# Performance work log

Measured on AMD Instinct MI355X. Metric: run time of the kernel, lower is better.

Reference implementation:

```python
import jax, jax.numpy as jnp
import numpy as np

FFT_LIST = [32, 64, 128]
C_IN = 64
C_OUT = 96
C_OUT_PER = C_OUT // len(FFT_LIST)  # 32
BASIC = FFT_LIST[1]                 # base kernel defined at fft=64 -> 33 bins
ALPHA = 0.2                         # tf.nn.leaky_relu default


def setup_inputs() -> dict:
    key = jax.random.key(0)
    k1, k2, k3, k4 = jax.random.split(key, 4)
    B, T = 8, 8192
    bins0 = BASIC // 2 + 1
    return {
        "x": jax.random.normal(k1, (B, T, C_IN), dtype=jnp.float32),
        "kernel_r": jax.random.normal(k2, (1, 1, bins0, C_IN * C_OUT_PER), dtype=jnp.float32) * 0.05,
        "kernel_i": jax.random.normal(k3, (1, 1, bins0, C_IN * C_OUT_PER), dtype=jnp.float32) * 0.05,
        "bias_r": jax.random.normal(k4, (C_OUT,), dtype=jnp.float32) * 0.05,
    }


def _resize_bins(k, bins):
    # tf.image.resize on [1, H=1, W=bins0, C]: bilinear along W, half-pixel, no antialias
    if bins == k.shape[2]:
        return k
    return jax.image.resize(k, (1, 1, bins, k.shape[3]), method="linear", antialias=False)


def _leaky(v):
    return jax.nn.leaky_relu(v, negative_slope=ALPHA)


def reference(x, kernel_r, kernel_i, bias_r):
    B, T, _ = x.shape
    xc = jnp.transpose(x, (0, 2, 1))  # [B, C_in, T]
    outs = []
    for fft_n in FFT_LIST:
        frames = T // fft_n
        bins = fft_n // 2 + 1
        # non-overlapping STFT with no window == reshape + rfft
        xf = jnp.fft.rfft(xc.reshape(B, C_IN, frames, fft_n), axis=-1)  # [B, Cin, F, K] complex64
        kr = _resize_bins(kernel_r, bins)
        ki = _resize_bins(kernel_i, bins)
        kern = (kr + 1j * ki).reshape(bins, C_IN, C_OUT_PER).astype(jnp.complex64)  # [K, Cin, Cout]
        # per-frequency-bin complex matmul over c_in (fuses tile+mul+reduce_sum)
        y = jnp.einsum("bcfk,kco->bofk", xf, kern)  # [B, Cout, F, K]
        # act_domain == 'freq': leaky relu on real and imag parts
        y = _leaky(jnp.real(y)) + 1j * _leaky(jnp.imag(y))
        # inverse STFT (step == length, no window) == irfft + reshape
        yt = jnp.fft.irfft(y, n=fft_n, axis=-1)            # [B, Cout, F, fft_n]
        yt = yt.reshape(B, C_OUT_PER, T)                    # [B, Cout, T]
        outs.append(jnp.transpose(yt, (0, 2, 1)))           # [B, T, Cout]
    out = jnp.concatenate(outs, axis=2)                     # [B, T, C_OUT]
    out = out + bias_r                                      # bias_add(real(bias))
    return out
```

## Files before the change

kernel.cpp:

```cpp
#include <hip/hip_runtime.h>
#include <stdint.h>

#define T_SZ 8192
#define NCH 96

typedef __attribute__((ext_vector_type(8))) short s8v;
typedef __attribute__((ext_vector_type(4))) float f4v;

__device__ __forceinline__ float lo_bf(uint32_t u){ return __uint_as_float(u << 16); }
__device__ __forceinline__ float hi_bf(uint32_t u){ return __uint_as_float(u & 0xffff0000u); }
__device__ __forceinline__ uint32_t f2bf(float f){
    uint32_t u = __float_as_uint(f);
    return (u + 0x7fffu + ((u >> 16) & 1u)) >> 16;
}
__device__ __forceinline__ uint32_t pk2(float a, float b){ return f2bf(a) | (f2bf(b) << 16); }

#define WS_TOTAL_PAIRS 235520
#define WD_OFF   942080
#define WD_ELEMS 27264
#define WA_OFF   996608
#define WA_ELEMS 30464
#define WD64_U16  1920
#define WD128_U16 7680
#define WA64_U16  2304
#define WA128_U16 8960
#define SLOT_A   1114112
#define SLOT_C  10485760
#define WS_PIPE 14942208
#define XF32W   1114112
#define XF64W  10485760
#define XF128W 19398656
#define Y32W   28311552
#define Y64W   32768000
#define Y128W  37224448
#define WS_WIDE 41484288

__global__ void prep_full(const float* __restrict__ kr, const float* __restrict__ ki,
                          char* __restrict__ ws)
{
    int idx = blockIdx.x * 256 + threadIdx.x;
    if (idx < WS_TOTAL_PAIRS) {
        int bins, rem = idx;
        if (rem < 17 * 2048)      { bins = 17; }
        else if (rem < 50 * 2048) { bins = 33; rem -= 17 * 2048; }
        else                      { bins = 65; rem -= 50 * 2048; }
        int k = rem >> 11, co = rem & 2047;
        float s  = (k + 0.5f) * (33.0f / bins) - 0.5f;
        float fl = floorf(s);
        float w1 = s - fl;
        int i0 = min(max((int)fl, 0), 32);
        int i1 = min(max((int)fl + 1, 0), 32);
        float r0 = kr[i0 * 2048 + co], r1 = kr[i1 * 2048 + co];
        float q0 = ki[i0 * 2048 + co], q1 = ki[i1 * 2048 + co];
        ((uint32_t*)ws)[idx] = pk2(fmaf(w1, r1 - r0, r0), fmaf(w1, q1 - q0, q0));
        return;
    }
    int e = idx - WS_TOTAL_PAIRS;
    if (e < WD_ELEMS) {
        int N, NP, base;
        if (e < 1920)      { N = 32;  NP = 40;  base = 0; }
        else if (e < 7680) { N = 64;  NP = 72;  base = WD64_U16;  e -= 1920; }
        else               { N = 128; NP = 136; base = WD128_U16; e -= 7680; }
        int m = e / NP, t = e % NP;
        float v = 0.f;
        if (t < N && m < N + 2) {
            float ang = 6.2831853071795864769f * (float)(((m >> 1) * t) & (N - 1)) / (float)N;
            v = (m & 1) ? -sinf(ang) : cosf(ang);
        }
        ((unsigned short*)(ws + WD_OFF))[base + e] = (unsigned short)f2bf(v);
        return;
    }
    e -= WD_ELEMS;
    if (e < WA_ELEMS) {
        int N, S3, base;
        if (e < 2304)      { N = 32;  S3 = 72;  base = 0; }
        else if (e < 8960) { N = 64;  S3 = 104; base = WA64_U16;  e -= 2304; }
        else               { N = 128; S3 = 168; base = WA128_U16; e -= 8960; }
        int t = e / S3, kk = e % S3;
        int BINS = N / 2 + 1;
        float v = 0.f;
        if (kk < BINS) {
            v = cosf(6.2831853071795864769f * (float)((kk * t) & (N - 1)) / (float)N);
        } else if (kk < N + 2) {
            v = -sinf(6.2831853071795864769f * (float)(((kk - BINS) * t) & (N - 1)) / (float)N);
        }
        ((unsigned short*)(ws + WA_OFF))[base + e] = (unsigned short)f2bf(v);
    }
}

__global__ void prep_resize(const float* __restrict__ kr, const float* __restrict__ ki,
                            uint32_t* __restrict__ wsu)
{
    int idx = blockIdx.x * 256 + threadIdx.x;
    if (idx >= WS_TOTAL_PAIRS) return;
    int bins, rem = idx;
    if (rem < 17 * 2048)      { bins = 17; }
    else if (rem < 50 * 2048) { bins = 33; rem -= 17 * 2048; }
    else                      { bins = 65; rem -= 50 * 2048; }
    int k = rem >> 11, co = rem & 2047;
    float s  = (k + 0.5f) * (33.0f / bins) - 0.5f;
    float fl = floorf(s);
    float w1 = s - fl;
    int i0 = min(max((int)fl, 0), 32);
    int i1 = min(max((int)fl + 1, 0), 32);
    float r0 = kr[i0 * 2048 + co], r1 = kr[i1 * 2048 + co];
    float q0 = ki[i0 * 2048 + co], q1 = ki[i1 * 2048 + co];
    wsu[idx] = pk2(fmaf(w1, r1 - r0, r0), fmaf(w1, q1 - q0, q0));
}

__device__ __forceinline__ s8v ldfr(const unsigned short* p, int stride, int row0, int k0){
    int lane = threadIdx.x & 63;
    return *(const s8v*)(p + (row0 + (lane & 15)) * stride + k0 + ((lane >> 4) << 3));
}

template<int N, int F>
__device__ __forceinline__ void k1_body(int bid, char* smem, const float* __restrict__ x,
        const unsigned short* __restrict__ WD, uint32_t* __restrict__ xfp)
{
    constexpr int BINS = N/2+1, FRAMES = 8192/N, BF = 8*FRAMES;
    constexpr int M2 = 2*BINS, MPAD = ((M2+15)/16)*16, NP = N+8;
    constexpr int COLS = F*64, NTT = COLS/16, NTW = NTT/4, MT = MPAD/16, KS = N/32;
    constexpr int BPB = FRAMES/F;

    unsigned short* W  = (unsigned short*)smem;
    unsigned short* xT = W + MPAD*NP;
    const int tid = threadIdx.x;
    const int b = bid / BPB, g = bid % BPB, f0 = g*F;

    for (int e = tid; e < MPAD*NP/8; e += 256)
        *(uint4*)(W + e*8) = *(const uint4*)(WD + e*8);

    const float* xb = x + ((size_t)b*T_SZ + (size_t)f0*N) * 64;
    for (int e = tid; e < F*N*4; e += 256) {
        int c4 = e & 15, q = e >> 4, s = q*4;
        const float* p = xb + (size_t)s*64 + c4*4;
        float4 v0 = *(const float4*)(p);
        float4 v1 = *(const float4*)(p + 64);
        float4 v2 = *(const float4*)(p + 128);
        float4 v3 = *(const float4*)(p + 192);
        int f = s / N, tq = s % N;
        unsigned short* d = xT + (f*64 + c4*4)*NP + tq;
        *(uint2*)(d)        = make_uint2(pk2(v0.x, v1.x), pk2(v2.x, v3.x));
        *(uint2*)(d + NP)   = make_uint2(pk2(v0.y, v1.y), pk2(v2.y, v3.y));
        *(uint2*)(d + 2*NP) = make_uint2(pk2(v0.z, v1.z), pk2(v2.z, v3.z));
        *(uint2*)(d + 3*NP) = make_uint2(pk2(v0.w, v1.w), pk2(v2.w, v3.w));
    }
    __syncthreads();

    const int wv = tid >> 6, lane = tid & 63;
    const int nt0 = wv * NTW, cl = lane & 15, rg = (lane >> 4) * 4;
    f4v acc[MT][NTW];
    #pragma unroll
    for (int mt = 0; mt < MT; ++mt)
        #pragma unroll
        for (int nw = 0; nw < NTW; ++nw) { f4v zz = {0.f,0.f,0.f,0.f}; acc[mt][nw] = zz; }

    for (int ks = 0; ks < KS; ++ks) {
        s8v a[MT];
        #pragma unroll
        for (int mt = 0; mt < MT; ++mt) a[mt] = ldfr(W, NP, mt*16, ks*32);
        #pragma unroll
        for (int nw = 0; nw < NTW; ++nw) {
            s8v bb = ldfr(xT, NP, (nt0+nw)*16, ks*32);
            #pragma unroll
            for (int mt = 0; mt < MT; ++mt)
                acc[mt][nw] = __builtin_amdgcn_mfma_f32_16x16x32_bf16(a[mt], bb, acc[mt][nw], 0, 0, 0);
        }
    }
    #pragma unroll
    for (int mt = 0; mt < MT; ++mt)
      #pragma unroll
      for (int nw = 0; nw < NTW; ++nw) {
        int col = (nt0+nw)*16 + cl, f = col >> 6, c = col & 63;
        size_t bf = (size_t)b*FRAMES + f0 + f;
        #pragma unroll
        for (int r = 0; r < 4; r += 2) {
            int m = mt*16 + rg + r, k = m >> 1;
            if (k < BINS)
                xfp[((size_t)k*BF + bf)*64 + c] = pk2(acc[mt][nw][r], acc[mt][nw][r+1]);
        }
      }
}

template<int N, int NTW>
__device__ __forceinline__ void k1w_branch(const unsigned short* __restrict__ W,
        const unsigned short* __restrict__ xT, uint32_t* __restrict__ xfp, int b, int w)
{
    constexpr int BINS = N/2+1, M2 = 2*BINS, MPAD = ((M2+15)/16)*16;
    constexpr int MT = MPAD/16, KS = N/32, NP = N+8;
    constexpr int F = 128/N, FRAMES = 8192/N, BF = 8*FRAMES;
    const int tid = threadIdx.x, wv = tid >> 6, lane = tid & 63;
    const int nt0 = wv * NTW, cl = lane & 15, kl = (lane >> 4) << 3, rg = (lane >> 4) * 4;

    f4v acc[MT][NTW];
    #pragma unroll
    for (int mt = 0; mt < MT; ++mt)
        #pragma unroll
        for (int nw = 0; nw < NTW; ++nw) { f4v zz = {0.f,0.f,0.f,0.f}; acc[mt][nw] = zz; }

    for (int ks = 0; ks < KS; ++ks) {
        s8v a[MT];
        #pragma unroll
        for (int mt = 0; mt < MT; ++mt) a[mt] = ldfr(W, NP, mt*16, ks*32);
        #pragma unroll
        for (int nw = 0; nw < NTW; ++nw) {
            int rowb = (nt0+nw)*16 + cl;
            s8v bb = *(const s8v*)(xT + (rowb & 63)*136 + (rowb >> 6)*N + ks*32 + kl);
            #pragma unroll
            for (int mt = 0; mt < MT; ++mt)
                acc[mt][nw] = __builtin_amdgcn_mfma_f32_16x16x32_bf16(a[mt], bb, acc[mt][nw], 0, 0, 0);
        }
    }
    #pragma unroll
    for (int mt = 0; mt < MT; ++mt)
      #pragma unroll
      for (int nw = 0; nw < NTW; ++nw) {
        int col = (nt0+nw)*16 + cl, f = col >> 6, c = col & 63;
        size_t bf = (size_t)b*FRAMES + w*F + f;
        #pragma unroll
        for (int r = 0; r < 4; r += 2) {
            int m = mt*16 + rg + r, k = m >> 1;
            if (k < BINS)
                xfp[((size_t)k*BF + bf)*64 + c] = pk2(acc[mt][nw][r], acc[mt][nw][r+1]);
        }
      }
}

__global__ __launch_bounds__(256) void k1w(const float* __restrict__ x, char* __restrict__ ws)
{
    __shared__ __align__(16) char smem[71936];
    unsigned short* xT   = (unsigned short*)smem;
    unsigned short* Wall = xT + 64*136;
    const unsigned short* WD = (const unsigned short*)(ws + WD_OFF);
    const int tid = threadIdx.x, bid = blockIdx.x;
    const int b = bid >> 6, w = bid & 63;

    for (int e = tid; e < WD_ELEMS/8; e += 256)
        *(uint4*)(Wall + e*8) = *(const uint4*)(WD + e*8);

    const float* xb = x + ((size_t)b*T_SZ + (size_t)w*128) * 64;
    for (int e = tid; e < 512; e += 256) {
        int c4 = e & 15, t0 = (e >> 4) * 4;
        const float* p = xb + (size_t)t0*64 + c4*4;
        float4 v0 = *(const float4*)(p);
        float4 v1 = *(const float4*)(p + 64);
        float4 v2 = *(const float4*)(p + 128);
        float4 v3 = *(const float4*)(p + 192);
        unsigned short* d = xT + (c4*4)*136 + t0;
        *(uint2*)(d)         = make_uint2(pk2(v0.x, v1.x), pk2(v2.x, v3.x));
        *(uint2*)(d + 136)   = make_uint2(pk2(v0.y, v1.y), pk2(v2.y, v3.y));
        *(uint2*)(d + 272)   = make_uint2(pk2(v0.z, v1.z), pk2(v2.z, v3.z));
        *(uint2*)(d + 408)   = make_uint2(pk2(v0.w, v1.w), pk2(v2.w, v3.w));
    }
    __syncthreads();

    k1w_branch<32, 4>(Wall,                          xT, (uint32_t*)(ws + XF32W),  b, w);
    k1w_branch<64, 2>(Wall + WD64_U16,               xT, (uint32_t*)(ws + XF64W),  b, w);
    k1w_branch<128,1>(Wall + WD128_U16,              xT, (uint32_t*)(ws + XF128W), b, w);
}

template<int N>
__device__ __forceinline__ void k2_body(int kbin, int mblk, char* smem,
        const uint32_t* __restrict__ wpair, const uint32_t* __restrict__ xfp,
        unsigned short* __restrict__ y2)
{
    constexpr int BINS = N/2+1, FRAMES = 8192/N, BF = 8*FRAMES, M2 = 2*BINS;
    unsigned short* A  = (unsigned short*)smem;
    unsigned short* W2 = A + 128*136;
    const int tid = threadIdx.x;
    const int bf0 = mblk * 128;

    for (int e = tid; e < 2048; e += 256)
        *(uint4*)(A + (e>>4)*136 + (e&15)*8) =
            *((const uint4*)(xfp + ((size_t)kbin*BF + bf0 + (e>>4))*64) + (e & 15));

    for (int e = tid; e < 2048; e += 256) {
        uint32_t pr = wpair[kbin*2048 + e];
        unsigned short krv = (unsigned short)(pr & 0xffffu);
        unsigned short kiv = (unsigned short)(pr >> 16);
        int c = e >> 5, o = e & 31;
        W2[o*136 + 2*c]          = krv;
        W2[o*136 + 2*c + 1]      = (unsigned short)(kiv ^ 0x8000u);
        W2[(32+o)*136 + 2*c]     = kiv;
        W2[(32+o)*136 + 2*c + 1] = krv;
    }
    __syncthreads();

    const int wv = tid >> 6, lane = tid & 63;
    const int mt0 = wv * 2;
    f4v acc[2][4];
    #pragma unroll
    for (int mt = 0; mt < 2; ++mt)
        #pragma unroll
        for (int nt = 0; nt < 4; ++nt) { f4v zz = {0.f,0.f,0.f,0.f}; acc[mt][nt] = zz; }

    for (int ks = 0; ks < 4; ++ks) {
        s8v a0 = ldfr(A, 136, mt0*16, ks*32);
        s8v a1 = ldfr(A, 136, mt0*16 + 16, ks*32);
        #pragma unroll
        for (int nt = 0; nt < 4; ++nt) {
            s8v bb = ldfr(W2, 136, nt*16, ks*32);
            acc[0][nt] = __builtin_amdgcn_mfma_f32_16x16x32_bf16(a0, bb, acc[0][nt], 0, 0, 0);
            acc[1][nt] = __builtin_amdgcn_mfma_f32_16x16x32_bf16(a1, bb, acc[1][nt], 0, 0, 0);
        }
    }
    const float wk = (kbin == 0 || kbin == BINS-1) ? (1.0f/N) : (2.0f/N);
    const int cl = lane & 15, rg = (lane >> 4) * 4;
    #pragma unroll
    for (int mt = 0; mt < 2; ++mt)
      #pragma unroll
      for (int nt = 0; nt < 4; ++nt) {
        int col = nt*16 + cl;
        int kk = (col < 32) ? kbin : BINS + kbin;
        int o = col & 31;
        #pragma unroll
        for (int r = 0; r < 4; ++r) {
            int bf = bf0 + (mt0+mt)*16 + rg + r;
            float v = acc[mt][nt][r];
            v = (v > 0.f) ? v : 0.2f * v;
            y2[((size_t)bf*M2 + kk)*32 + o] = (unsigned short)f2bf(v * wk);
        }
      }
}

template<int N>
__device__ __forceinline__ void k3_body(int bid, char* smem,
        const unsigned short* __restrict__ WA, const unsigned short* __restrict__ y2,
        const float* __restrict__ bias, float* __restrict__ out)
{
    constexpr int BINS = N/2+1, FRAMES = 8192/N, M2 = 2*BINS;
    constexpr int KP = ((M2+31)/32)*32, S3 = KP+8;
    constexpr int FB = (N==32)?8:(N==64)?4:2, NCOLS = FB*32, KS = KP/32;
    constexpr int COFF = (N==32)?0:(N==64)?32:64;

    unsigned short* A  = (unsigned short*)smem;
    unsigned short* Bt = A + N*S3;
    const int tid = threadIdx.x;
    const int b = bid >> 5, fg = bid & 31, f0 = fg * FB;

    for (int e = tid; e < N*S3/8; e += 256)
        *(uint4*)(A + e*8) = *(const uint4*)(WA + e*8);

    for (int e = tid; e < FB*M2*4; e += 256) {
        int f = e / (M2*4), r = e % (M2*4), kk = r >> 2, og = (r & 3)*8;
        size_t bf = (size_t)b*FRAMES + f0 + f;
        uint4 v = *((const uint4*)(y2 + ((size_t)bf*M2 + kk)*32) + (r & 3));
        unsigned short* dst = Bt + (f*32 + og)*S3 + kk;
        const unsigned short* pv = (const unsigned short*)&v;
        #pragma unroll
        for (int j = 0; j < 8; ++j) dst[j*S3] = pv[j];
    }
    __syncthreads();

    const int wv = tid >> 6, lane = tid & 63;
    constexpr int MTW = (N==128)?2:1;
    constexpr int NTW = (N==128)?4:8;
    const int mt0 = (N==128) ? wv*2 : ((N==32) ? (wv & 1) : wv);
    const int nt0 = (N==32) ? (wv >> 1)*8 : 0;

    f4v acc[MTW][NTW];
    #pragma unroll
    for (int i = 0; i < MTW; ++i)
        #pragma unroll
        for (int nw = 0; nw < NTW; ++nw) { f4v zz = {0.f,0.f,0.f,0.f}; acc[i][nw] = zz; }

    for (int ks = 0; ks < KS; ++ks) {
        s8v a[MTW];
        #pragma unroll
        for (int i = 0; i < MTW; ++i) a[i] = ldfr(A, S3, (mt0+i)*16, ks*32);
        #pragma unroll
        for (int nw = 0; nw < NTW; ++nw) {
            s8v bb = ldfr(Bt, S3, (nt0+nw)*16, ks*32);
            #pragma unroll
            for (int i = 0; i < MTW; ++i)
                acc[i][nw] = __builtin_amdgcn_mfma_f32_16x16x32_bf16(a[i], bb, acc[i][nw], 0, 0, 0);
        }
    }
    const int cl = lane & 15, rg = (lane >> 4) * 4;
    #pragma unroll
    for (int nw = 0; nw < NTW; ++nw) {
        int col = (nt0+nw)*16 + cl, f = col >> 5, o = col & 31;
        float bv = bias[COFF + o];
        #pragma unroll
        for (int i = 0; i < MTW; ++i)
            #pragma unroll
            for (int r = 0; r < 4; ++r) {
                int t = (mt0+i)*16 + rg + r;
                out[((size_t)(b*T_SZ + (f0+f)*N + t))*NCH + COFF + o] = acc[i][nw][r] + bv;
            }
    }
}

__global__ __launch_bounds__(256) void k1s32(const float* __restrict__ x, char* __restrict__ ws)
{
    __shared__ __align__(16) char smem[24320];
    k1_body<32,4>(blockIdx.x, smem, x, (const unsigned short*)(ws + WD_OFF),
                  (uint32_t*)(ws + SLOT_A));
}
template<int N>
__global__ __launch_bounds__(256) void k2s(char* __restrict__ ws)
{
    __shared__ __align__(16) char smem[52224];
    constexpr int MB = (8192/N*8)/128;
    constexpr int WSP = (N==32) ? 0 : (N==64) ? 17*2048 : 50*2048;
    k2_body<N>(blockIdx.x / MB, blockIdx.x % MB, smem, (const uint32_t*)ws + WSP,
               (const uint32_t*)(ws + SLOT_A), (unsigned short*)(ws + SLOT_C));
}
__global__ __launch_bounds__(256) void k3s128(char* __restrict__ ws,
        const float* __restrict__ bias, float* __restrict__ out)
{
    __shared__ __align__(16) char smem[64512];
    k3_body<128>(blockIdx.x, smem, (const unsigned short*)(ws + WA_OFF) + WA128_U16,
                 (const unsigned short*)(ws + SLOT_C), bias, out);
}
__global__ __launch_bounds__(256) void mix32(const float* __restrict__ x, char* __restrict__ ws,
        const float* __restrict__ bias, float* __restrict__ out)
{
    __shared__ __align__(16) char smem[48384];
    int bid = blockIdx.x;
    if (bid < 256)
        k3_body<32>(bid, smem, (const unsigned short*)(ws + WA_OFF),
                    (const unsigned short*)(ws + SLOT_C), bias, out);
    else
        k1_body<64,4>(bid - 256, smem, x, (const unsigned short*)(ws + WD_OFF) + WD64_U16,
                      (uint32_t*)(ws + SLOT_A));
}
__global__ __launch_bounds__(256) void mix64(const float* __restrict__ x, char* __restrict__ ws,
        const float* __restrict__ bias, float* __restrict__ out)
{
    __shared__ __align__(16) char smem[73984];
    int bid = blockIdx.x;
    if (bid < 256)
        k3_body<64>(bid, smem, (const unsigned short*)(ws + WA_OFF) + WA64_U16,
                    (const unsigned short*)(ws + SLOT_C), bias, out);
    else
        k1_body<128,2>(bid - 256, smem, x, (const unsigned short*)(ws + WD_OFF) + WD128_U16,
                       (uint32_t*)(ws + SLOT_A));
}
__global__ __launch_bounds__(256) void k2all(char* __restrict__ ws)
{
    __shared__ __align__(16) char smem[52224];
    int bid = blockIdx.x;
    if (bid < 272)
        k2_body<32>(bid >> 4, bid & 15, smem, (const uint32_t*)ws,
                    (const uint32_t*)(ws + XF32W), (unsigned short*)(ws + Y32W));
    else if (bid < 536) {
        int q = bid - 272;
        k2_body<64>(q >> 3, q & 7, smem, (const uint32_t*)ws + 17*2048,
                    (const uint32_t*)(ws + XF64W), (unsigned short*)(ws + Y64W));
    } else {
        int q = bid - 536;
        k2_body<128>(q >> 2, q & 3, smem, (const uint32_t*)ws + 50*2048,
                     (const uint32_t*)(ws + XF128W), (unsigned short*)(ws + Y128W));
    }
}
__global__ __launch_bounds__(256) void k3all(char* __restrict__ ws,
        const float* __restrict__ bias, float* __restrict__ out)
{
    __shared__ __align__(16) char smem[64512];
    int bid = blockIdx.x;
    if (bid < 256)
        k3_body<32>(bid, smem, (const unsigned short*)(ws + WA_OFF),
                    (const unsigned short*)(ws + Y32W), bias, out);
    else if (bid < 512)
        k3_body<64>(bid - 256, smem, (const unsigned short*)(ws + WA_OFF) + WA64_U16,
                    (const unsigned short*)(ws + Y64W), bias, out);
    else
        k3_body<128>(bid - 512, smem, (const unsigned short*)(ws + WA_OFF) + WA128_U16,
                     (const unsigned short*)(ws + Y128W), bias, out);
}

template<int FFT_N, bool USE_WS>
__global__ __launch_bounds__(256, 2)
void stft_fused(const float* __restrict__ x, const float* __restrict__ kr,
                const float* __restrict__ ki, const float* __restrict__ bias,
                const uint32_t* __restrict__ wsu, float* __restrict__ out)
{
    constexpr int CIN = 64, COUT = 32;
    constexpr int BINS = FFT_N / 2 + 1;
    constexpr int NFR  = 128 / FFT_N;
    constexpr int KQ   = (BINS + 3) / 4;
    constexpr int COFF = (FFT_N == 32) ? 0 : (FFT_N == 64) ? 32 : 64;
    constexpr int WSP  = (FFT_N == 32) ? 0 : (FFT_N == 64) ? 17 * 2048 : 50 * 2048;
    constexpr int XSP  = 68;
    constexpr int CP   = 66;
    constexpr int YP   = BINS + 2;
    constexpr int SMEMF = 128 * XSP + 2 * FFT_N + NFR * BINS * CP * 2;

    __shared__ __align__(16) float smem[SMEMF];
    float*  xs  = smem;
    float2* cst = (float2*)(smem + 128 * XSP);
    float2* xf2 = (float2*)(smem + 128 * XSP + 2 * FFT_N);
    float2* Y2  = (float2*)smem;

    const int tid = threadIdx.x;
    const int bid = blockIdx.x;
    const int b = bid >> 6, w = bid & 63;
    const float* xblk = x + (size_t)(b * T_SZ + w * 128) * CIN;

    for (int i = tid; i < 2048; i += 256) {
        float4 v = ((const float4*)xblk)[i];
        int t = i >> 4;
        int c = (i & 15) * 4;
        *(float4*)&xs[t * XSP + c] = v;
    }
    if (tid < FFT_N) {
        float ang = 6.2831853071795864769f * ((float)tid / (float)FFT_N);
        float sv, cv;
        sincosf(ang, &sv, &cv);
        cst[tid] = make_float2(cv, sv);
    }
    __syncthreads();

    constexpr int NT_DFT = NFR * KQ * 16;
    for (int tile = tid; tile < NT_DFT; tile += 256) {
        int cq  = tile & 15;
        int kqf = tile >> 4;
        int kq  = kqf % KQ, f = kqf / KQ;
        int k0  = kq * 4;
        float accr[4][4] = {};
        float acci[4][4] = {};
        int idx[4] = {0, 0, 0, 0};
        const float* xrow = xs + f * FFT_N * XSP + cq * 4;
        for (int t = 0; t < FFT_N; ++t) {
            float4 xv = *(const float4*)(xrow + t * XSP);
            float xc[4] = {xv.x, xv.y, xv.z, xv.w};
            #pragma unroll
            for (int kk = 0; kk < 4; ++kk) {
                float2 tw = cst[idx[kk]];
                idx[kk] = (idx[kk] + k0 + kk) & (FFT_N - 1);
                #pragma unroll
                for (int cc = 0; cc < 4; ++cc) {
                    accr[kk][cc] = fmaf(xc[cc], tw.x, accr[kk][cc]);
                    acci[kk][cc] = fmaf(xc[cc], tw.y, acci[kk][cc]);
                }
            }
        }
        #pragma unroll
        for (int kk = 0; kk < 4; ++kk) {
            int k = k0 + kk;
            if (k < BINS) {
                #pragma unroll
                for (int cc = 0; cc < 4; ++cc)
                    xf2[(f * BINS + k) * CP + cq * 4 + cc] =
                        make_float2(accr[kk][cc], -acci[kk][cc]);
            }
        }
    }
    __syncthreads();

    constexpr int NT_MM = BINS * 8;
    for (int task = tid; task < NT_MM; task += 256) {
        int oq = task & 7, k = task >> 3;
        float2 accY[NFR][4] = {};
        float w1 = 0.f; int i0 = 0, i1 = 0;
        if (!USE_WS) {
            float s  = (k + 0.5f) * (33.0f / BINS) - 0.5f;
            float fl = floorf(s); w1 = s - fl;
            i0 = min(max((int)fl, 0), 32);
            i1 = min(max((int)fl + 1, 0), 32);
        }
        const uint32_t* wp = USE_WS ? (wsu + WSP + k * 2048 + oq * 4) : (const uint32_t*)nullptr;
        for (int c = 0; c < CIN; ++c) {
            float krv[4], kiv[4];
            if (USE_WS) {
                uint4 u = *(const uint4*)(wp + c * 32);
                krv[0] = lo_bf(u.x); kiv[0] = hi_bf(u.x);
                krv[1] = lo_bf(u.y); kiv[1] = hi_bf(u.y);
                krv[2] = lo_bf(u.z); kiv[2] = hi_bf(u.z);
                krv[3] = lo_bf(u.w); kiv[3] = hi_bf(u.w);
            } else {
                const float* p = kr + (size_t)i0 * 2048 + c * 32 + oq * 4;
                const float* q = kr + (size_t)i1 * 2048 + c * 32 + oq * 4;
                float4 r0 = *(const float4*)p, r1 = *(const float4*)q;
                p = ki + (size_t)i0 * 2048 + c * 32 + oq * 4;
                q = ki + (size_t)i1 * 2048 + c * 32 + oq * 4;
                float4 q0 = *(const float4*)p, q1 = *(const float4*)q;
                krv[0] = fmaf(w1, r1.x - r0.x, r0.x); kiv[0] = fmaf(w1, q1.x - q0.x, q0.x);
                krv[1] = fmaf(w1, r1.y - r0.y, r0.y); kiv[1] = fmaf(w1, q1.y - q0.y, q0.y);
                krv[2] = fmaf(w1, r1.z - r0.z, r0.z); kiv[2] = fmaf(w1, q1.z - q0.z, q0.z);
                krv[3] = fmaf(w1, r1.w - r0.w, r0.w); kiv[3] = fmaf(w1, q1.w - q0.w, q0.w);
            }
            #pragma unroll
            for (int f = 0; f < NFR; ++f) {
                float2 xv = xf2[(f * BINS + k) * CP + c];
                #pragma unroll
                for (int jo = 0; jo < 4; ++jo) {
                    accY[f][jo].x += xv.x * krv[jo] - xv.y * kiv[jo];
                    accY[f][jo].y += xv.x * kiv[jo] + xv.y * krv[jo];
                }
            }
        }
        float wk = (k == 0 || k == BINS - 1) ? (1.0f / FFT_N) : (2.0f / FFT_N);
        #pragma unroll
        for (int f = 0; f < NFR; ++f) {
            #pragma unroll
            for (int jo = 0; jo < 4; ++jo) {
                float yr = accY[f][jo].x; yr = (yr > 0.f) ? yr : 0.2f * yr;
                float yi = accY[f][jo].y; yi = (yi > 0.f) ? yi : 0.2f * yi;
                Y2[(f * COUT + oq * 4 + jo) * YP + k] = make_float2(yr * wk, yi * wk);
            }
        }
    }
    __syncthreads();

    {
        int tq = tid >> 3, oq = tid & 7;
        int tg0 = tq * 4;
        int f   = tg0 / FFT_N;
        int tl0 = tg0 % FFT_N;
        float acc[4][4] = {};
        int idx[4] = {0, 0, 0, 0};
        const float2* yb = Y2 + (f * COUT + oq * 4) * YP;
        for (int k = 0; k < BINS; ++k) {
            float2 tw[4];
            #pragma unroll
            for (int j = 0; j < 4; ++j) {
                tw[j] = cst[idx[j]];
                idx[j] = (idx[j] + tl0 + j) & (FFT_N - 1);
            }
            #pragma unroll
            for (int jo = 0; jo < 4; ++jo) {
                float2 yv = yb[jo * YP + k];
                #pragma unroll
                for (int j = 0; j < 4; ++j)
                    acc[j][jo] += yv.x * tw[j].x - yv.y * tw[j].y;
            }
        }
        float4 bv = *(const float4*)(bias + COFF + oq * 4);
        float* ob = out + ((size_t)(b * T_SZ + w * 128 + tg0)) * NCH + COFF + oq * 4;
        #pragma unroll
        for (int j = 0; j < 4; ++j) {
            float4 o4 = make_float4(acc[j][0] + bv.x, acc[j][1] + bv.y,
                                    acc[j][2] + bv.z, acc[j][3] + bv.w);
            *(float4*)(ob + (size_t)j * NCH) = o4;
        }
    }
}

extern "C" void kernel_launch(void* const* d_in, const int* in_sizes, int n_in,
                              void* d_out, int out_size, void* d_ws, size_t ws_size,
                              hipStream_t stream)
{
    (void)in_sizes; (void)n_in; (void)out_size;
    const float* x    = (const float*)d_in[0];
    const float* kr   = (const float*)d_in[1];
    const float* ki   = (const float*)d_in[2];
    const float* bias = (const float*)d_in[3];
    float* out = (float*)d_out;
    char* ws = (char*)d_ws;
    dim3 blk(256);

    if (ws != nullptr && ws_size >= (size_t)WS_WIDE) {
        prep_full<<<dim3(1146), blk, 0, stream>>>(kr, ki, ws);
        k1w   <<<dim3(512), blk, 0, stream>>>(x, ws);
        k2all <<<dim3(796), blk, 0, stream>>>(ws);
        k3all <<<dim3(768), blk, 0, stream>>>(ws, bias, out);
    } else if (ws != nullptr && ws_size >= (size_t)WS_PIPE) {
        prep_full<<<dim3(1146), blk, 0, stream>>>(kr, ki, ws);
        k1s32   <<<dim3(512), blk, 0, stream>>>(x, ws);
        k2s<32> <<<dim3(272), blk, 0, stream>>>(ws);
        mix32   <<<dim3(512), blk, 0, stream>>>(x, ws, bias, out);
        k2s<64> <<<dim3(264), blk, 0, stream>>>(ws);
        mix64   <<<dim3(512), blk, 0, stream>>>(x, ws, bias, out);
        k2s<128><<<dim3(260), blk, 0, stream>>>(ws);
        k3s128  <<<dim3(256), blk, 0, stream>>>(ws, bias, out);
    } else if (ws != nullptr && ws_size >= (size_t)WS_TOTAL_PAIRS * 4) {
        uint32_t* wsu = (uint32_t*)ws;
        prep_resize<<<dim3(920), blk, 0, stream>>>(kr, ki, wsu);
        stft_fused<32,  true><<<dim3(512), blk, 0, stream>>>(x, kr, ki, bias, wsu, out);
        stft_fused<64,  true><<<dim3(512), blk, 0, stream>>>(x, kr, ki, bias, wsu, out);
        stft_fused<128, true><<<dim3(512), blk, 0, stream>>>(x, kr, ki, bias, wsu, out);
    } else {
        stft_fused<32,  false><<<dim3(512), blk, 0, stream>>>(x, kr, ki, bias, nullptr, out);
        stft_fused<64,  false><<<dim3(512), blk, 0, stream>>>(x, kr, ki, bias, nullptr, out);
        stft_fused<128, false><<<dim3(512), blk, 0, stream>>>(x, kr, ki, bias, nullptr, out);
    }
}
```

Before: 49.05 us.

## Pre-expand complex weights into GEMM layout, split k3 N=128 tiles, add occupancy bounds

Measured after the change: 50.37 us. 1.03x slower.

```diff
diff --git a/kernel.cpp b/kernel.cpp
--- a/kernel.cpp
+++ b/kernel.cpp
@@ -16,46 +16,52 @@
 __device__ __forceinline__ uint32_t pk2(float a, float b){ return f2bf(a) | (f2bf(b) << 16); }
 
 #define WS_TOTAL_PAIRS 235520
-#define WD_OFF   942080
-#define WD_ELEMS 27264
-#define WA_OFF   996608
-#define WA_ELEMS 30464
-#define WD64_U16  1920
-#define WD128_U16 7680
-#define WA64_U16  2304
-#define WA128_U16 8960
-#define SLOT_A   1114112
-#define SLOT_C  10485760
-#define WS_PIPE 14942208
-#define XF32W   1114112
-#define XF64W  10485760
-#define XF128W 19398656
-#define Y32W   28311552
-#define Y64W   32768000
-#define Y128W  37224448
-#define WS_WIDE 41484288
+#define WD_OFF    942080
+#define WD_ELEMS  27264
+#define WA_OFF    996608
+#define WA_ELEMS  30464
+#define WD64_U16   1920
+#define WD128_U16  7680
+#define WA64_U16   2304
+#define WA128_U16  8960
+#define WE_OFF   1057536
+#define WE_U32    471040
+#define XF32W    4194304
+#define XF64W   14680064
+#define XF128W  25165824
+#define Y32W    35651584
+#define Y64W    41943040
+#define Y128W   50331648
+#define WS_WIDE 58720256
 
 __global__ void prep_full(const float* __restrict__ kr, const float* __restrict__ ki,
                           char* __restrict__ ws)
 {
     int idx = blockIdx.x * 256 + threadIdx.x;
-    if (idx < WS_TOTAL_PAIRS) {
-        int bins, rem = idx;
-        if (rem < 17 * 2048)      { bins = 17; }
-        else if (rem < 50 * 2048) { bins = 33; rem -= 17 * 2048; }
-        else                      { bins = 65; rem -= 50 * 2048; }
-        int k = rem >> 11, co = rem & 2047;
+    if (idx < WE_U32) {
+        int g = idx >> 12, r = idx & 4095;
+        int row = r >> 6, c = r & 63;
+        int o = row & 31, half = row >> 5;
+        int bins, k;
+        if (g < 17)      { bins = 17; k = g; }
+        else if (g < 50) { bins = 33; k = g - 17; }
+        else             { bins = 65; k = g - 50; }
         float s  = (k + 0.5f) * (33.0f / bins) - 0.5f;
         float fl = floorf(s);
         float w1 = s - fl;
         int i0 = min(max((int)fl, 0), 32);
         int i1 = min(max((int)fl + 1, 0), 32);
+        int co = c * 32 + o;
         float r0 = kr[i0 * 2048 + co], r1 = kr[i1 * 2048 + co];
         float q0 = ki[i0 * 2048 + co], q1 = ki[i1 * 2048 + co];
-        ((uint32_t*)ws)[idx] = pk2(fmaf(w1, r1 - r0, r0), fmaf(w1, q1 - q0, q0));
+        int N = bins * 2 - 2;
+        float wk = (k == 0 || k == bins - 1) ? (1.0f / N) : (2.0f / N);
+        float vr = fmaf(w1, r1 - r0, r0) * wk;
+        float vi = fmaf(w1, q1 - q0, q0) * wk;
+        ((uint32_t*)(ws + WE_OFF))[idx] = half ? pk2(vi, vr) : pk2(vr, -vi);
         return;
     }
-    int e = idx - WS_TOTAL_PAIRS;
+    int e = idx - WE_U32;
     if (e < WD_ELEMS) {
         int N, NP, base;
         if (e < 1920)      { N = 32;  NP = 40;  base = 0; }
@@ -79,11 +85,10 @@
         int t = e / S3, kk = e % S3;
         int BINS = N / 2 + 1;
         float v = 0.f;
-        if (kk < BINS) {
+        if (kk < BINS)
             v = cosf(6.2831853071795864769f * (float)((kk * t) & (N - 1)) / (float)N);
-        } else if (kk < N + 2) {
+        else if (kk < N + 2)
             v = -sinf(6.2831853071795864769f * (float)(((kk - BINS) * t) & (N - 1)) / (float)N);
-        }
         ((unsigned short*)(ws + WA_OFF))[base + e] = (unsigned short)f2bf(v);
     }
 }
@@ -113,75 +118,6 @@
     return *(const s8v*)(p + (row0 + (lane & 15)) * stride + k0 + ((lane >> 4) << 3));
 }
 
-template<int N, int F>
-__device__ __forceinline__ void k1_body(int bid, char* smem, const float* __restrict__ x,
-        const unsigned short* __restrict__ WD, uint32_t* __restrict__ xfp)
-{
-    constexpr int BINS = N/2+1, FRAMES = 8192/N, BF = 8*FRAMES;
-    constexpr int M2 = 2*BINS, MPAD = ((M2+15)/16)*16, NP = N+8;
-    constexpr int COLS = F*64, NTT = COLS/16, NTW = NTT/4, MT = MPAD/16, KS = N/32;
-    constexpr int BPB = FRAMES/F;
-
-    unsigned short* W  = (unsigned short*)smem;
-    unsigned short* xT = W + MPAD*NP;
-    const int tid = threadIdx.x;
-    const int b = bid / BPB, g = bid % BPB, f0 = g*F;
-
-    for (int e = tid; e < MPAD*NP/8; e += 256)
-        *(uint4*)(W + e*8) = *(const uint4*)(WD + e*8);
-
-    const float* xb = x + ((size_t)b*T_SZ + (size_t)f0*N) * 64;
-    for (int e = tid; e < F*N*4; e += 256) {
-        int c4 = e & 15, q = e >> 4, s = q*4;
-        const float* p = xb + (size_t)s*64 + c4*4;
-        float4 v0 = *(const float4*)(p);
-        float4 v1 = *(const float4*)(p + 64);
-        float4 v2 = *(const float4*)(p + 128);
-        float4 v3 = *(const float4*)(p + 192);
-        int f = s / N, tq = s % N;
-        unsigned short* d = xT + (f*64 + c4*4)*NP + tq;
-        *(uint2*)(d)        = make_uint2(pk2(v0.x, v1.x), pk2(v2.x, v3.x));
-        *(uint2*)(d + NP)   = make_uint2(pk2(v0.y, v1.y), pk2(v2.y, v3.y));
-        *(uint2*)(d + 2*NP) = make_uint2(pk2(v0.z, v1.z), pk2(v2.z, v3.z));
-        *(uint2*)(d + 3*NP) = make_uint2(pk2(v0.w, v1.w), pk2(v2.w, v3.w));
-    }
-    __syncthreads();
-
-    const int wv = tid >> 6, lane = tid & 63;
-    const int nt0 = wv * NTW, cl = lane & 15, rg = (lane >> 4) * 4;
-    f4v acc[MT][NTW];
-    #pragma unroll
-    for (int mt = 0; mt < MT; ++mt)
-        #pragma unroll
-        for (int nw = 0; nw < NTW; ++nw) { f4v zz = {0.f,0.f,0.f,0.f}; acc[mt][nw] = zz; }
-
-    for (int ks = 0; ks < KS; ++ks) {
-        s8v a[MT];
-        #pragma unroll
-        for (int mt = 0; mt < MT; ++mt) a[mt] = ldfr(W, NP, mt*16, ks*32);
-        #pragma unroll
-        for (int nw = 0; nw < NTW; ++nw) {
-            s8v bb = ldfr(xT, NP, (nt0+nw)*16, ks*32);
-            #pragma unroll
-            for (int mt = 0; mt < MT; ++mt)
-                acc[mt][nw] = __builtin_amdgcn_mfma_f32_16x16x32_bf16(a[mt], bb, acc[mt][nw], 0, 0, 0);
-        }
-    }
-    #pragma unroll
-    for (int mt = 0; mt < MT; ++mt)
-      #pragma unroll
-      for (int nw = 0; nw < NTW; ++nw) {
-        int col = (nt0+nw)*16 + cl, f = col >> 6, c = col & 63;
-        size_t bf = (size_t)b*FRAMES + f0 + f;
-        #pragma unroll
-        for (int r = 0; r < 4; r += 2) {
-            int m = mt*16 + rg + r, k = m >> 1;
-            if (k < BINS)
-                xfp[((size_t)k*BF + bf)*64 + c] = pk2(acc[mt][nw][r], acc[mt][nw][r+1]);
-        }
-      }
-}
-
 template<int N, int NTW>
 __device__ __forceinline__ void k1w_branch(const unsigned short* __restrict__ W,
         const unsigned short* __restrict__ xT, uint32_t* __restrict__ xfp, int b, int w)
@@ -226,7 +162,7 @@
       }
 }
 
-__global__ __launch_bounds__(256) void k1w(const float* __restrict__ x, char* __restrict__ ws)
+__global__ __launch_bounds__(256, 2) void k1w(const float* __restrict__ x, char* __restrict__ ws)
 {
     __shared__ __align__(16) char smem[71936];
     unsigned short* xT   = (unsigned short*)smem;
@@ -247,24 +183,25 @@
         float4 v2 = *(const float4*)(p + 128);
         float4 v3 = *(const float4*)(p + 192);
         unsigned short* d = xT + (c4*4)*136 + t0;
-        *(uint2*)(d)         = make_uint2(pk2(v0.x, v1.x), pk2(v2.x, v3.x));
-        *(uint2*)(d + 136)   = make_uint2(pk2(v0.y, v1.y), pk2(v2.y, v3.y));
-        *(uint2*)(d + 272)   = make_uint2(pk2(v0.z, v1.z), pk2(v2.z, v3.z));
-        *(uint2*)(d + 408)   = make_uint2(pk2(v0.w, v1.w), pk2(v2.w, v3.w));
+        *(uint2*)(d)       = make_uint2(pk2(v0.x, v1.x), pk2(v2.x, v3.x));
+        *(uint2*)(d + 136) = make_uint2(pk2(v0.y, v1.y), pk2(v2.y, v3.y));
+        *(uint2*)(d + 272) = make_uint2(pk2(v0.z, v1.z), pk2(v2.z, v3.z));
+        *(uint2*)(d + 408) = make_uint2(pk2(v0.w, v1.w), pk2(v2.w, v3.w));
     }
     __syncthreads();
 
-    k1w_branch<32, 4>(Wall,                          xT, (uint32_t*)(ws + XF32W),  b, w);
-    k1w_branch<64, 2>(Wall + WD64_U16,               xT, (uint32_t*)(ws + XF64W),  b, w);
-    k1w_branch<128,1>(Wall + WD128_U16,              xT, (uint32_t*)(ws + XF128W), b, w);
+    k1w_branch<32, 4>(Wall,             xT, (uint32_t*)(ws + XF32W),  b, w);
+    k1w_branch<64, 2>(Wall + WD64_U16,  xT, (uint32_t*)(ws + XF64W),  b, w);
+    k1w_branch<128,1>(Wall + WD128_U16, xT, (uint32_t*)(ws + XF128W), b, w);
 }
 
 template<int N>
 __device__ __forceinline__ void k2_body(int kbin, int mblk, char* smem,
-        const uint32_t* __restrict__ wpair, const uint32_t* __restrict__ xfp,
+        const unsigned short* __restrict__ we, const uint32_t* __restrict__ xfp,
         unsigned short* __restrict__ y2)
 {
     constexpr int BINS = N/2+1, FRAMES = 8192/N, BF = 8*FRAMES, M2 = 2*BINS;
+    constexpr int GOFF = (N==32) ? 0 : (N==64) ? 17 : 50;
     unsigned short* A  = (unsigned short*)smem;
     unsigned short* W2 = A + 128*136;
     const int tid = threadIdx.x;
@@ -274,16 +211,9 @@
         *(uint4*)(A + (e>>4)*136 + (e&15)*8) =
             *((const uint4*)(xfp + ((size_t)kbin*BF + bf0 + (e>>4))*64) + (e & 15));
 
-    for (int e = tid; e < 2048; e += 256) {
-        uint32_t pr = wpair[kbin*2048 + e];
-        unsigned short krv = (unsigned short)(pr & 0xffffu);
-        unsigned short kiv = (unsigned short)(pr >> 16);
-        int c = e >> 5, o = e & 31;
-        W2[o*136 + 2*c]          = krv;
-        W2[o*136 + 2*c + 1]      = (unsigned short)(kiv ^ 0x8000u);
-        W2[(32+o)*136 + 2*c]     = kiv;
-        W2[(32+o)*136 + 2*c + 1] = krv;
-    }
+    const uint4* wsrc = (const uint4*)(we + (size_t)(GOFF + kbin) * 8192);
+    for (int e = tid; e < 1024; e += 256)
+        *(uint4*)(W2 + (e>>4)*136 + (e&15)*8) = wsrc[e];
     __syncthreads();
 
     const int wv = tid >> 6, lane = tid & 63;
@@ -304,7 +234,6 @@
             acc[1][nt] = __builtin_amdgcn_mfma_f32_16x16x32_bf16(a1, bb, acc[1][nt], 0, 0, 0);
         }
     }
-    const float wk = (kbin == 0 || kbin == BINS-1) ? (1.0f/N) : (2.0f/N);
     const int cl = lane & 15, rg = (lane >> 4) * 4;
     #pragma unroll
     for (int mt = 0; mt < 2; ++mt)
@@ -318,28 +247,47 @@
             int bf = bf0 + (mt0+mt)*16 + rg + r;
             float v = acc[mt][nt][r];
             v = (v > 0.f) ? v : 0.2f * v;
-            y2[((size_t)bf*M2 + kk)*32 + o] = (unsigned short)f2bf(v * wk);
+            y2[((size_t)bf*M2 + kk)*32 + o] = (unsigned short)f2bf(v);
         }
       }
 }
 
-template<int N>
-__device__ __forceinline__ void k3_body(int bid, char* smem,
+__global__ __launch_bounds__(256, 3) void k2all(char* __restrict__ ws)
+{
+    __shared__ __align__(16) char smem[52224];
+    const unsigned short* we = (const unsigned short*)(ws + WE_OFF);
+    int bid = blockIdx.x;
+    if (bid < 272)
+        k2_body<32>(bid >> 4, bid & 15, smem, we,
+                    (const uint32_t*)(ws + XF32W), (unsigned short*)(ws + Y32W));
+    else if (bid < 536) {
+        int q = bid - 272;
+        k2_body<64>(q >> 3, q & 7, smem, we,
+                    (const uint32_t*)(ws + XF64W), (unsigned short*)(ws + Y64W));
+    } else {
+        int q = bid - 536;
+        k2_body<128>(q >> 2, q & 3, smem, we,
+                     (const uint32_t*)(ws + XF128W), (unsigned short*)(ws + Y128W));
+    }
+}
+
+template<int N, int TROWS>
+__device__ __forceinline__ void k3_body(int b, int f0, int t0, char* smem,
         const unsigned short* __restrict__ WA, const unsigned short* __restrict__ y2,
         const float* __restrict__ bias, float* __restrict__ out)
 {
     constexpr int BINS = N/2+1, FRAMES = 8192/N, M2 = 2*BINS;
-    constexpr int KP = ((M2+31)/32)*32, S3 = KP+8;
-    constexpr int FB = (N==32)?8:(N==64)?4:2, NCOLS = FB*32, KS = KP/32;
+    constexpr int KP = ((M2+31)/32)*32, S3 = KP+8, KS = KP/32;
+    constexpr int FB = (N==32)?8:(N==64)?4:2;
     constexpr int COFF = (N==32)?0:(N==64)?32:64;
+    constexpr int NTW = (N==128)?4:8;
 
     unsigned short* A  = (unsigned short*)smem;
-    unsigned short* Bt = A + N*S3;
+    unsigned short* Bt = A + TROWS*S3;
     const int tid = threadIdx.x;
-    const int b = bid >> 5, fg = bid & 31, f0 = fg * FB;
-
-    for (int e = tid; e < N*S3/8; e += 256)
-        *(uint4*)(A + e*8) = *(const uint4*)(WA + e*8);
+
+    for (int e = tid; e < TROWS*S3/8; e += 256)
+        *(uint4*)(A + e*8) = *(const uint4*)(WA + t0*S3 + e*8);
 
     for (int e = tid; e < FB*M2*4; e += 256) {
         int f = e / (M2*4), r = e % (M2*4), kk = r >> 2, og = (r & 3)*8;
@@ -353,27 +301,19 @@
     __syncthreads();
 
     const int wv = tid >> 6, lane = tid & 63;
-    constexpr int MTW = (N==128)?2:1;
-    constexpr int NTW = (N==128)?4:8;
-    const int mt0 = (N==128) ? wv*2 : ((N==32) ? (wv & 1) : wv);
+    const int mt0 = (N==32) ? (wv & 1) : wv;
     const int nt0 = (N==32) ? (wv >> 1)*8 : 0;
 
-    f4v acc[MTW][NTW];
+    f4v acc[NTW];
     #pragma unroll
-    for (int i = 0; i < MTW; ++i)
-        #pragma unroll
-        for (int nw = 0; nw < NTW; ++nw) { f4v zz = {0.f,0.f,0.f,0.f}; acc[i][nw] = zz; }
+    for (int nw = 0; nw < NTW; ++nw) { f4v zz = {0.f,0.f,0.f,0.f}; acc[nw] = zz; }
 
     for (int ks = 0; ks < KS; ++ks) {
-        s8v a[MTW];
-        #pragma unroll
-        for (int i = 0; i < MTW; ++i) a[i] = ldfr(A, S3, (mt0+i)*16, ks*32);
+        s8v a = ldfr(A, S3, mt0*16, ks*32);
         #pragma unroll
         for (int nw = 0; nw < NTW; ++nw) {
             s8v bb = ldfr(Bt, S3, (nt0+nw)*16, ks*32);
-            #pragma unroll
-            for (int i = 0; i < MTW; ++i)
-                acc[i][nw] = __builtin_amdgcn_mfma_f32_16x16x32_bf16(a[i], bb, acc[i][nw], 0, 0, 0);
+            acc[nw] = __builtin_amdgcn_mfma_f32_16x16x32_bf16(a, bb, acc[nw], 0, 0, 0);
         }
     }
     const int cl = lane & 15, rg = (lane >> 4) * 4;
@@ -382,92 +322,31 @@
         int col = (nt0+nw)*16 + cl, f = col >> 5, o = col & 31;
         float bv = bias[COFF + o];
         #pragma unroll
-        for (int i = 0; i < MTW; ++i)
-            #pragma unroll
-            for (int r = 0; r < 4; ++r) {
-                int t = (mt0+i)*16 + rg + r;
-                out[((size_t)(b*T_SZ + (f0+f)*N + t))*NCH + COFF + o] = acc[i][nw][r] + bv;
-            }
-    }
-}
-
-__global__ __launch_bounds__(256) void k1s32(const float* __restrict__ x, char* __restrict__ ws)
-{
-    __shared__ __align__(16) char smem[24320];
-    k1_body<32,4>(blockIdx.x, smem, x, (const unsigned short*)(ws + WD_OFF),
-                  (uint32_t*)(ws + SLOT_A));
-}
-template<int N>
-__global__ __launch_bounds__(256) void k2s(char* __restrict__ ws)
-{
-    __shared__ __align__(16) char smem[52224];
-    constexpr int MB = (8192/N*8)/128;
-    constexpr int WSP = (N==32) ? 0 : (N==64) ? 17*2048 : 50*2048;
-    k2_body<N>(blockIdx.x / MB, blockIdx.x % MB, smem, (const uint32_t*)ws + WSP,
-               (const uint32_t*)(ws + SLOT_A), (unsigned short*)(ws + SLOT_C));
-}
-__global__ __launch_bounds__(256) void k3s128(char* __restrict__ ws,
+        for (int r = 0; r < 4; ++r) {
+            int t = t0 + mt0*16 + rg + r;
+            out[((size_t)(b*T_SZ + (f0+f)*N + t))*NCH + COFF + o] = acc[nw][r] + bv;
+        }
+    }
+}
+
+__global__ __launch_bounds__(256, 3) void k3all(char* __restrict__ ws,
         const float* __restrict__ bias, float* __restrict__ out)
 {
-    __shared__ __align__(16) char smem[64512];
-    k3_body<128>(blockIdx.x, smem, (const unsigned short*)(ws + WA_OFF) + WA128_U16,
-                 (const unsigned short*)(ws + SLOT_C), bias, out);
-}
-__global__ __launch_bounds__(256) void mix32(const float* __restrict__ x, char* __restrict__ ws,
-        const float* __restrict__ bias, float* __restrict__ out)
-{
-    __shared__ __align__(16) char smem[48384];
+    __shared__ __align__(16) char smem[43008];
+    const unsigned short* WA = (const unsigned short*)(ws + WA_OFF);
     int bid = blockIdx.x;
     if (bid < 256)
-        k3_body<32>(bid, smem, (const unsigned short*)(ws + WA_OFF),
-                    (const unsigned short*)(ws + SLOT_C), bias, out);
-    else
-        k1_body<64,4>(bid - 256, smem, x, (const unsigned short*)(ws + WD_OFF) + WD64_U16,
-                      (uint32_t*)(ws + SLOT_A));
-}
-__global__ __launch_bounds__(256) void mix64(const float* __restrict__ x, char* __restrict__ ws,
-        const float* __restrict__ bias, float* __restrict__ out)
-{
-    __shared__ __align__(16) char smem[73984];
-    int bid = blockIdx.x;
-    if (bid < 256)
-        k3_body<64>(bid, smem, (const unsigned short*)(ws + WA_OFF) + WA64_U16,
-                    (const unsigned short*)(ws + SLOT_C), bias, out);
-    else
-        k1_body<128,2>(bid - 256, smem, x, (const unsigned short*)(ws + WD_OFF) + WD128_U16,
-                       (uint32_t*)(ws + SLOT_A));
-}
-__global__ __launch_bounds__(256) void k2all(char* __restrict__ ws)
-{
-    __shared__ __align__(16) char smem[52224];
-    int bid = blockIdx.x;
-    if (bid < 272)
-        k2_body<32>(bid >> 4, bid & 15, smem, (const uint32_t*)ws,
-                    (const uint32_t*)(ws + XF32W), (unsigned short*)(ws + Y32W));
-    else if (bid < 536) {
-        int q = bid - 272;
-        k2_body<64>(q >> 3, q & 7, smem, (const uint32_t*)ws + 17*2048,
-                    (const uint32_t*)(ws + XF64W), (unsigned short*)(ws + Y64W));
+        k3_body<32,32>(bid >> 5, (bid & 31)*8, 0, smem, WA,
+                       (const unsigned short*)(ws + Y32W), bias, out);
+    else if (bid < 512) {
+        int q = bid - 256;
+        k3_body<64,64>(q >> 5, (q & 31)*4, 0, smem, WA + WA64_U16,
+                       (const unsigned short*)(ws + Y64W), bias, out);
     } else {
-        int q = bid - 536;
-        k2_body<128>(q >> 2, q & 3, smem, (const uint32_t*)ws + 50*2048,
-                     (const uint32_t*)(ws + XF128W), (unsigned short*)(ws + Y128W));
-    }
-}
-__global__ __launch_bounds__(256) void k3all(char* __restrict__ ws,
-        const float* __restrict__ bias, float* __restrict__ out)
-{
-    __shared__ __align__(16) char smem[64512];
-    int bid = blockIdx.x;
-    if (bid < 256)
-        k3_body<32>(bid, smem, (const unsigned short*)(ws + WA_OFF),
-                    (const unsigned short*)(ws + Y32W), bias, out);
-    else if (bid < 512)
-        k3_body<64>(bid - 256, smem, (const unsigned short*)(ws + WA_OFF) + WA64_U16,
-                    (const unsigned short*)(ws + Y64W), bias, out);
-    else
-        k3_body<128>(bid - 512, smem, (const unsigned short*)(ws + WA_OFF) + WA128_U16,
-                     (const unsigned short*)(ws + Y128W), bias, out);
+        int q = bid - 512;
+        k3_body<128,64>(q >> 6, ((q & 63) >> 1)*2, (q & 1)*64, smem, WA + WA128_U16,
+                        (const unsigned short*)(ws + Y128W), bias, out);
+    }
 }
 
 template<int FFT_N, bool USE_WS>
@@ -652,19 +531,10 @@
     dim3 blk(256);
 
     if (ws != nullptr && ws_size >= (size_t)WS_WIDE) {
-        prep_full<<<dim3(1146), blk, 0, stream>>>(kr, ki, ws);
-        k1w   <<<dim3(512), blk, 0, stream>>>(x, ws);
-        k2all <<<dim3(796), blk, 0, stream>>>(ws);
-        k3all <<<dim3(768), blk, 0, stream>>>(ws, bias, out);
-    } else if (ws != nullptr && ws_size >= (size_t)WS_PIPE) {
-        prep_full<<<dim3(1146), blk, 0, stream>>>(kr, ki, ws);
-        k1s32   <<<dim3(512), blk, 0, stream>>>(x, ws);
-        k2s<32> <<<dim3(272), blk, 0, stream>>>(ws);
-        mix32   <<<dim3(512), blk, 0, stream>>>(x, ws, bias, out);
-        k2s<64> <<<dim3(264), blk, 0, stream>>>(ws);
-        mix64   <<<dim3(512), blk, 0, stream>>>(x, ws, bias, out);
-        k2s<128><<<dim3(260), blk, 0, stream>>>(ws);
-        k3s128  <<<dim3(256), blk, 0, stream>>>(ws, bias, out);
+        prep_full<<<dim3(2066), blk, 0, stream>>>(kr, ki, ws);
+        k1w   <<<dim3(512),  blk, 0, stream>>>(x, ws);
+        k2all <<<dim3(796),  blk, 0, stream>>>(ws);
+        k3all <<<dim3(1024), blk, 0, stream>>>(ws, bias, out);
     } else if (ws != nullptr && ws_size >= (size_t)WS_TOTAL_PAIRS * 4) {
         uint32_t* wsu = (uint32_t*)ws;
         prep_resize<<<dim3(920), blk, 0, stream>>>(kr, ki, wsu);
```
